# Optimization experiments

Measured on AMD Instinct MI355X. Metric: run time of the kernel, lower is better.

## Reference

```python
import jax, jax.numpy as jnp
import numpy as np

I_DECAY = 0.95
STAG_THRESH = 0.95
MAX_GATE = 0.6
MIN_I_GATE = 0.25
EPS = 1e-12


def setup_inputs() -> dict:
    key = jax.random.key(0)
    ks = jax.random.split(key, 9)
    B, T, D_IN, D_OUT = 4, 2048, 2048, 2048
    x = jax.random.normal(ks[0], (B, T, D_IN), dtype=jnp.float32)
    s = 1.0 / np.sqrt(D_IN)
    Wp = jax.random.uniform(ks[1], (D_IN, D_OUT), jnp.float32, -s, s)
    Wi = jax.random.uniform(ks[2], (D_IN, D_OUT), jnp.float32, -s, s) * 0.3
    Wd = jax.random.uniform(ks[3], (D_IN, D_OUT), jnp.float32, -s, s) * 0.3
    gate_w = jax.random.uniform(ks[4], (D_IN, 3), jnp.float32, -s, s)
    gate_b = jnp.array([0.5, 0.0, 0.0], dtype=jnp.float32)
    kick_vec = jax.random.normal(ks[5], (D_OUT,), dtype=jnp.float32) * 0.01
    kick_w = jax.random.uniform(ks[6], (D_IN, 1), jnp.float32, -s, s)
    kick_b = jnp.full((1,), -2.0, dtype=jnp.float32)
    bias = jnp.zeros((D_OUT,), dtype=jnp.float32)
    return {"x": x, "Wp": Wp, "Wi": Wi, "Wd": Wd, "gate_w": gate_w,
            "gate_b": gate_b, "kick_vec": kick_vec, "kick_w": kick_w,
            "kick_b": kick_b, "bias": bias}


def _ema_integral(x, decay):
    # x: [B,T,D] -> time-major scan; integral[0] = x[0]
    xt = jnp.swapaxes(x, 0, 1)  # [T,B,D]

    def step(carry, xcur):
        new = decay * carry + (1.0 - decay) * xcur
        return new, new

    init = xt[0]
    _, rest = jax.lax.scan(step, init, xt[1:])
    integral = jnp.concatenate([init[None], rest], axis=0)
    return jnp.swapaxes(integral, 0, 1)  # [B,T,D]


def reference(x, Wp, Wi, Wd, gate_w, gate_b, kick_vec, kick_w, kick_b, bias):
    B, T, D = x.shape
    # --- EMA integral (linear recurrence over T) ---
    integral = _ema_integral(x, I_DECAY)

    # --- stagnation-aware derivative ---
    diff = jnp.concatenate(
        [jnp.zeros_like(x[:, :1]), x[:, 1:] - x[:, :-1]], axis=1)
    x_norm = x / jnp.maximum(
        jnp.linalg.norm(x, axis=-1, keepdims=True), EPS)
    cos_sim = jnp.concatenate(
        [jnp.zeros((B, 1), x.dtype),
         jnp.sum(x_norm[:, 1:] * x_norm[:, :-1], axis=-1)], axis=1)  # [B,T]
    stagnation = (cos_sim > STAG_THRESH).astype(x.dtype)
    kick_strength = jax.nn.sigmoid(
        jnp.einsum('btd,do->bto', x, kick_w) + kick_b)[..., 0]  # [B,T]
    derivative = diff + (stagnation * kick_strength)[..., None] * kick_vec

    # --- gates: softmax -> clamp max -> clamp I min -> renormalize ---
    g = jax.nn.softmax(jnp.einsum('btd,dg->btg', x, gate_w) + gate_b, axis=-1)
    g = jnp.minimum(g, MAX_GATE)
    g = g.at[..., 1].set(jnp.maximum(g[..., 1], MIN_I_GATE))
    g = g / jnp.sum(g, axis=-1, keepdims=True)

    out = (g[..., 0:1] * jnp.einsum('btd,do->bto', x, Wp)
           + g[..., 1:2] * jnp.einsum('btd,do->bto', integral, Wi)
           + g[..., 2:3] * jnp.einsum('btd,do->bto', derivative, Wd))
    return out + bias
```

## Files before the change

### kernel.cpp

```cpp
#include <hip/hip_runtime.h>

#define DH 2048
#define TT 2048
#define BB 4
#define MROWS 8192
#define NZ 6144
#define NCH 128
#define LCH 16
#define LAM 0.44012667f
#define LAM2 1.982646e-06f

typedef __attribute__((ext_vector_type(8))) short bf16x8;
typedef __attribute__((ext_vector_type(4))) float f32x4;

__device__ __forceinline__ unsigned short f2bf(float f) {
  union { float f; unsigned int u; } v; v.f = f;
  unsigned int u = v.u;
  return (unsigned short)((u + 0x7FFFu + ((u >> 16) & 1u)) >> 16);
}
__device__ __forceinline__ float bf2f(unsigned short u) {
  union { unsigned int i; float f; } v; v.i = ((unsigned int)u) << 16;
  return v.f;
}
__device__ __forceinline__ void gld16(const unsigned short* g, unsigned short* l) {
  __builtin_amdgcn_global_load_lds((const __attribute__((address_space(1))) void*)g,
                                   (__attribute__((address_space(3))) void*)l, 16, 0, 0);
}

__global__ __launch_bounds__(256) void prep_w(const float* __restrict__ Wp,
                                              const float* __restrict__ Wi,
                                              const float* __restrict__ Wd,
                                              const float* __restrict__ kick_vec,
                                              unsigned short* __restrict__ Wt,
                                              float* __restrict__ kvWd) {
  __shared__ float tile[64][65];
  int bid = blockIdx.x;
  int mat = bid >> 10;
  int t2 = bid & 1023;
  int dt = (t2 >> 5) * 64;
  int ot = (t2 & 31) * 64;
  const float* W = (mat == 0) ? Wp : ((mat == 1) ? Wi : Wd);
  int nbase = mat * DH;
  int tid = threadIdx.x;
  int r = tid >> 4;
  int c4 = (tid & 15) * 4;
#pragma unroll
  for (int i = 0; i < 4; ++i) {
    int rr = r + i * 16;
    float4 v = *(const float4*)&W[(size_t)(dt + rr) * DH + ot + c4];
    tile[rr][c4 + 0] = v.x; tile[rr][c4 + 1] = v.y;
    tile[rr][c4 + 2] = v.z; tile[rr][c4 + 3] = v.w;
  }
  __syncthreads();
  int o = tid >> 3;
  int d8 = (tid & 7) * 8;
#pragma unroll
  for (int pass = 0; pass < 2; ++pass) {
    int oo = o + pass * 32;
    union { unsigned short u[8]; uint4 v; } pk;
#pragma unroll
    for (int i = 0; i < 8; ++i) pk.u[i] = f2bf(tile[d8 + i][oo]);
    *(uint4*)&Wt[(size_t)(nbase + ot + oo) * DH + dt + d8] = pk.v;
  }
  if (mat == 2 && tid < 64) {
    float s = 0.f;
#pragma unroll 8
    for (int dd = 0; dd < 64; ++dd) s += kick_vec[dt + dd] * tile[dd][tid];
    atomicAdd(&kvWd[ot + tid], s);
  }
}

__global__ __launch_bounds__(256) void conv_x(const float* __restrict__ x,
                                              const float* __restrict__ gate_w,
                                              const float* __restrict__ gate_b,
                                              const float* __restrict__ kick_w,
                                              const float* __restrict__ kick_b,
                                              float* __restrict__ rs,
                                              unsigned short* __restrict__ A) {
  int r = blockIdx.x;
  int t = r & (TT - 1);
  const float* xr = x + (size_t)r * DH;
  const float* xq = xr - DH;
  const bool hp = (t != 0);
  int tid = threadIdx.x;
  float a0 = 0, a1 = 0, a2 = 0, ak = 0, axx = 0, apx = 0, app = 0;
#pragma unroll
  for (int it = 0; it < 2; ++it) {
    int d0 = (tid + it * 256) * 4;
    float4 xv = *(const float4*)(xr + d0);
    float4 pv = hp ? *(const float4*)(xq + d0) : make_float4(0.f, 0.f, 0.f, 0.f);
    float4 q0 = *(const float4*)(gate_w + (size_t)d0 * 3);
    float4 q1 = *(const float4*)(gate_w + (size_t)d0 * 3 + 4);
    float4 q2 = *(const float4*)(gate_w + (size_t)d0 * 3 + 8);
    float4 kw = *(const float4*)(kick_w + d0);
    float xa[4] = {xv.x, xv.y, xv.z, xv.w};
    float pa[4] = {pv.x, pv.y, pv.z, pv.w};
    a0 += xa[0] * q0.x + xa[1] * q0.w + xa[2] * q1.z + xa[3] * q2.y;
    a1 += xa[0] * q0.y + xa[1] * q1.x + xa[2] * q1.w + xa[3] * q2.z;
    a2 += xa[0] * q0.z + xa[1] * q1.y + xa[2] * q2.x + xa[3] * q2.w;
    ak += xa[0] * kw.x + xa[1] * kw.y + xa[2] * kw.z + xa[3] * kw.w;
    union { unsigned short u[4]; uint2 v; } pk;
#pragma unroll
    for (int j = 0; j < 4; ++j) {
      axx += xa[j] * xa[j];
      apx += xa[j] * pa[j];
      app += pa[j] * pa[j];
      pk.u[j] = f2bf(xa[j]);
    }
    *(uint2*)&A[(size_t)r * DH + d0] = pk.v;
  }
#pragma unroll
  for (int off = 32; off > 0; off >>= 1) {
    a0 += __shfl_xor(a0, off); a1 += __shfl_xor(a1, off);
    a2 += __shfl_xor(a2, off); ak += __shfl_xor(ak, off);
    axx += __shfl_xor(axx, off); apx += __shfl_xor(apx, off);
    app += __shfl_xor(app, off);
  }
  __shared__ float red[4][7];
  int wv = tid >> 6;
  if ((tid & 63) == 0) {
    red[wv][0] = a0; red[wv][1] = a1; red[wv][2] = a2; red[wv][3] = ak;
    red[wv][4] = axx; red[wv][5] = apx; red[wv][6] = app;
  }
  __syncthreads();
  if (tid == 0) {
    float v[7];
#pragma unroll
    for (int i = 0; i < 7; ++i) v[i] = red[0][i] + red[1][i] + red[2][i] + red[3][i];
    float l0 = v[0] + gate_b[0], l1 = v[1] + gate_b[1], l2 = v[2] + gate_b[2];
    float mx = fmaxf(l0, fmaxf(l1, l2));
    float e0 = expf(l0 - mx), e1 = expf(l1 - mx), e2 = expf(l2 - mx);
    float inv = 1.f / (e0 + e1 + e2);
    float G0 = fminf(e0 * inv, 0.6f);
    float G1 = fminf(e1 * inv, 0.6f);
    float G2 = fminf(e2 * inv, 0.6f);
    G1 = fmaxf(G1, 0.25f);
    float inv2 = 1.f / (G0 + G1 + G2);
    G0 *= inv2; G1 *= inv2; G2 *= inv2;
    float ks = 1.f / (1.f + expf(-(v[3] + kick_b[0])));
    float nn = fmaxf(sqrtf(v[4]), 1e-12f) * fmaxf(sqrtf(v[6]), 1e-12f);
    float cs = hp ? (v[5] / nn) : 0.f;
    float cc = (cs > 0.95f) ? (G2 * ks) : 0.f;
    *(float4*)(rs + (size_t)r * 4) = make_float4(G0, G1, G2, cc);
  }
}

__global__ __launch_bounds__(256) void gemm_kernel(const unsigned short* __restrict__ A,
                                                   const unsigned short* __restrict__ Bt,
                                                   unsigned short* __restrict__ Z) {
  __shared__ __align__(16) unsigned short lA[128 * 64];
  __shared__ __align__(16) unsigned short lB[128 * 64];
  const int tid = threadIdx.x;
  const int wave = tid >> 6, lane = tid & 63;
  const int bid = blockIdx.x;
  const int xcd = bid & 7;
  const int loc = bid >> 3;
  const int mblk = xcd * 8 + (loc & 7);
  const int nblk = loc >> 3;
  const int m0 = mblk * 128, n0 = nblk * 128;

  const int srow = wave * 32 + (lane >> 3);
  const int scol = ((lane & 7) ^ (lane >> 3)) * 8;
  const unsigned short* ga = A + (size_t)(m0 + srow) * DH + scol;
  const unsigned short* gb = Bt + (size_t)(n0 + srow) * DH + scol;
  unsigned short* la = &lA[(wave * 32) * 64];
  unsigned short* lb = &lB[(wave * 32) * 64];

  f32x4 acc[4][4] = {};
  const int arow = ((wave >> 1) * 64 + (lane & 15)) * 64;
  const int brow = ((wave & 1) * 64 + (lane & 15)) * 64;
  const int cbq = lane >> 4;
  const int swz = lane & 7;

  for (int k0 = 0; k0 < DH; k0 += 64) {
#pragma unroll
    for (int j = 0; j < 4; ++j) {
      gld16(ga + k0 + (size_t)j * 8 * DH, la + j * 8 * 64);
      gld16(gb + k0 + (size_t)j * 8 * DH, lb + j * 8 * 64);
    }
    __syncthreads();
#pragma unroll
    for (int kb = 0; kb < 2; ++kb) {
      const int kphys = ((kb * 4 + cbq) ^ swz) * 8;
      bf16x8 av[4], bv[4];
#pragma unroll
      for (int mi = 0; mi < 4; ++mi)
        av[mi] = *(const bf16x8*)&lA[arow + mi * 16 * 64 + kphys];
#pragma unroll
      for (int ni = 0; ni < 4; ++ni)
        bv[ni] = *(const bf16x8*)&lB[brow + ni * 16 * 64 + kphys];
#pragma unroll
      for (int mi = 0; mi < 4; ++mi)
#pragma unroll
        for (int ni = 0; ni < 4; ++ni)
          acc[mi][ni] = __builtin_amdgcn_mfma_f32_16x16x32_bf16(av[mi], bv[ni], acc[mi][ni], 0, 0, 0);
    }
    __syncthreads();
  }

  const int lr = lane >> 4, lc = lane & 15;
  const int mbase = m0 + (wave >> 1) * 64, nbase = n0 + (wave & 1) * 64;
#pragma unroll
  for (int ni = 0; ni < 4; ++ni) {
    const int n = nbase + ni * 16 + lc;
#pragma unroll
    for (int mi = 0; mi < 4; ++mi) {
#pragma unroll
      for (int rg = 0; rg < 4; ++rg) {
        const int m = mbase + mi * 16 + lr * 4 + rg;
        Z[(size_t)m * NZ + n] = f2bf(acc[mi][ni][rg]);
      }
    }
  }
}

__global__ __launch_bounds__(256) void zi_carry(const unsigned short* __restrict__ Z,
                                                unsigned short* __restrict__ cpb) {
  int gid = blockIdx.x * 256 + threadIdx.x;
  int n = (gid & 511) * 4;
  int ch = (gid >> 9) & (NCH - 1);
  int b = gid >> 16;
  const unsigned short* zp = Z + ((size_t)(b * TT + ch * LCH)) * NZ + DH + n;
  float J0, J1, J2, J3;
  int tstart;
  if (ch == 0) {
    union { unsigned short u[4]; uint2 v; } c;
    c.v = *(const uint2*)zp;
    J0 = bf2f(c.u[0]); J1 = bf2f(c.u[1]); J2 = bf2f(c.u[2]); J3 = bf2f(c.u[3]);
    tstart = 1;
  } else {
    J0 = J1 = J2 = J3 = 0.f;
    tstart = 0;
  }
#pragma unroll 4
  for (int t = tstart; t < LCH; ++t) {
    union { unsigned short u[4]; uint2 v; } c;
    c.v = *(const uint2*)(zp + (size_t)t * NZ);
    J0 = 0.95f * J0 + 0.05f * bf2f(c.u[0]);
    J1 = 0.95f * J1 + 0.05f * bf2f(c.u[1]);
    J2 = 0.95f * J2 + 0.05f * bf2f(c.u[2]);
    J3 = 0.95f * J3 + 0.05f * bf2f(c.u[3]);
  }
  union { unsigned short u[4]; uint2 v; } o;
  o.u[0] = f2bf(J0); o.u[1] = f2bf(J1); o.u[2] = f2bf(J2); o.u[3] = f2bf(J3);
  *(uint2*)&cpb[((size_t)b * NCH + ch) * DH + n] = o.v;
}

__global__ __launch_bounds__(256) void zi_p1(unsigned short* __restrict__ cpb,
                                             float* __restrict__ gc) {
  int gid = blockIdx.x * 256 + threadIdx.x;
  int n = (gid & 511) * 4;
  int g = (gid >> 9) & 7;
  int b = gid >> 12;
  float r0 = 0, r1 = 0, r2 = 0, r3 = 0;
#pragma unroll
  for (int j = 0; j < 16; ++j) {
    size_t idx = ((size_t)b * NCH + g * 16 + j) * DH + n;
    union { unsigned short u[4]; uint2 v; } c;
    c.v = *(const uint2*)&cpb[idx];
    float c0 = bf2f(c.u[0]), c1 = bf2f(c.u[1]), c2 = bf2f(c.u[2]), c3 = bf2f(c.u[3]);
    union { unsigned short u[4]; uint2 v; } o;
    o.u[0] = f2bf(r0); o.u[1] = f2bf(r1); o.u[2] = f2bf(r2); o.u[3] = f2bf(r3);
    *(uint2*)&cpb[idx] = o.v;
    r0 = c0 + LAM * r0; r1 = c1 + LAM * r1;
    r2 = c2 + LAM * r2; r3 = c3 + LAM * r3;
  }
  *(float4*)&gc[((size_t)b * 8 + g) * DH + n] = make_float4(r0, r1, r2, r3);
}

__global__ __launch_bounds__(256) void zi_p2(float* __restrict__ gc) {
  int gid = blockIdx.x * 256 + threadIdx.x;
  int n = (gid & 511) * 4;
  int b = gid >> 9;
  float4 run = make_float4(0.f, 0.f, 0.f, 0.f);
#pragma unroll
  for (int g = 0; g < 8; ++g) {
    size_t idx = ((size_t)b * 8 + g) * DH + n;
    float4 old = *(const float4*)&gc[idx];
    *(float4*)&gc[idx] = run;
    run.x = old.x + LAM2 * run.x;
    run.y = old.y + LAM2 * run.y;
    run.z = old.z + LAM2 * run.z;
    run.w = old.w + LAM2 * run.w;
  }
}

__global__ __launch_bounds__(256) void final_combine(const unsigned short* __restrict__ Z,
                                                     const float* __restrict__ rs,
                                                     const unsigned short* __restrict__ cpb,
                                                     const float* __restrict__ gc,
                                                     const float* __restrict__ kvWd,
                                                     const float* __restrict__ bias,
                                                     float* __restrict__ out) {
  int tid = threadIdx.x;
  int n = tid * 8;
  int ch = blockIdx.x & (NCH - 1);
  int b = blockIdx.x >> 7;
  int r0 = b * TT + ch * LCH;
  const unsigned short* zb = Z + (size_t)r0 * NZ + n;
  const bool first_chunk = (ch == 0);

  int g = ch >> 4, j = ch & 15;
  float pw = 1.f;
  for (int i = 0; i < j; ++i) pw *= LAM;
  float Pv[8];
  {
    union { unsigned short u[8]; uint4 v; } c;
    c.v = *(const uint4*)&cpb[((size_t)b * NCH + ch) * DH + n];
    float4 gp0 = *(const float4*)&gc[((size_t)b * 8 + g) * DH + n];
    float4 gp1 = *(const float4*)&gc[((size_t)b * 8 + g) * DH + n + 4];
    float gp[8] = {gp0.x, gp0.y, gp0.z, gp0.w, gp1.x, gp1.y, gp1.z, gp1.w};
#pragma unroll
    for (int i = 0; i < 8; ++i) Pv[i] = bf2f(c.u[i]) + pw * gp[i];
  }
  float kv[8], bz[8];
  {
    float4 k0 = *(const float4*)&kvWd[n], k1 = *(const float4*)&kvWd[n + 4];
    float4 b0 = *(const float4*)&bias[n], b1 = *(const float4*)&bias[n + 4];
    kv[0]=k0.x; kv[1]=k0.y; kv[2]=k0.z; kv[3]=k0.w; kv[4]=k1.x; kv[5]=k1.y; kv[6]=k1.z; kv[7]=k1.w;
    bz[0]=b0.x; bz[1]=b0.y; bz[2]=b0.z; bz[3]=b0.w; bz[4]=b1.x; bz[5]=b1.y; bz[6]=b1.z; bz[7]=b1.w;
  }
  float zdp[8];
  if (!first_chunk) {
    union { unsigned short u[8]; uint4 v; } c;
    c.v = *(const uint4*)(zb - NZ + 2 * DH);
#pragma unroll
    for (int i = 0; i < 8; ++i) zdp[i] = bf2f(c.u[i]);
  } else {
#pragma unroll
    for (int i = 0; i < 8; ++i) zdp[i] = 0.f;
  }
  float J[8];
#pragma unroll
  for (int i = 0; i < 8; ++i) J[i] = 0.f;
  float f = 1.f;
  uint4 cp = *(const uint4*)(zb);
  uint4 ci = *(const uint4*)(zb + DH);
  uint4 cd = *(const uint4*)(zb + 2 * DH);
#pragma unroll
  for (int tau = 0; tau < LCH; ++tau) {
    uint4 np, ni, nd;
    if (tau < LCH - 1) {
      const unsigned short* zn = zb + (size_t)(tau + 1) * NZ;
      np = *(const uint4*)(zn);
      ni = *(const uint4*)(zn + DH);
      nd = *(const uint4*)(zn + 2 * DH);
    }
    float4 gg = *(const float4*)&rs[(size_t)(r0 + tau) * 4];
    union { unsigned short u[8]; uint4 v; } up, ui, ud;
    up.v = cp; ui.v = ci; ud.v = cd;
    const bool vfirst = first_chunk && (tau == 0);
    f *= 0.95f;
    float o[8];
#pragma unroll
    for (int i = 0; i < 8; ++i) {
      float xp = bf2f(up.u[i]), xi = bf2f(ui.u[i]), xd = bf2f(ud.u[i]);
      if (vfirst) J[i] = xi;
      else J[i] = 0.95f * J[i] + 0.05f * xi;
      float I = J[i] + f * Pv[i];
      float diff = vfirst ? 0.f : (xd - zdp[i]);
      o[i] = gg.x * xp + gg.y * I + gg.z * diff + gg.w * kv[i] + bz[i];
      zdp[i] = xd;
    }
    float* orow = out + (size_t)(r0 + tau) * DH + n;
    *(float4*)(orow) = make_float4(o[0], o[1], o[2], o[3]);
    *(float4*)(orow + 4) = make_float4(o[4], o[5], o[6], o[7]);
    cp = np; ci = ni; cd = nd;
  }
}

extern "C" void kernel_launch(void* const* d_in, const int* in_sizes, int n_in,
                              void* d_out, int out_size, void* d_ws, size_t ws_size,
                              hipStream_t stream) {
  const float* x        = (const float*)d_in[0];
  const float* Wp       = (const float*)d_in[1];
  const float* Wi       = (const float*)d_in[2];
  const float* Wd       = (const float*)d_in[3];
  const float* gate_w   = (const float*)d_in[4];
  const float* gate_b   = (const float*)d_in[5];
  const float* kick_vec = (const float*)d_in[6];
  const float* kick_w   = (const float*)d_in[7];
  const float* kick_b   = (const float*)d_in[8];
  const float* bias     = (const float*)d_in[9];
  float* out = (float*)d_out;

  char* ws = (char*)d_ws;
  unsigned short* Wt  = (unsigned short*)(ws + 0);
  unsigned short* Z   = (unsigned short*)(ws + 25165824);
  float* rs   = (float*)(ws + 125829120);
  float* kvWd = (float*)(ws + 125960192);
  unsigned short* cpb = (unsigned short*)(ws + 125968384);
  float* gc   = (float*)(ws + 128065536);
  unsigned short* A = (unsigned short*)d_out;
  (void)ws_size; (void)in_sizes; (void)n_in; (void)out_size;

  hipMemsetAsync(kvWd, 0, DH * sizeof(float), stream);
  prep_w<<<dim3(3072), dim3(256), 0, stream>>>(Wp, Wi, Wd, kick_vec, Wt, kvWd);
  conv_x<<<dim3(8192), dim3(256), 0, stream>>>(x, gate_w, gate_b, kick_w, kick_b, rs, A);
  gemm_kernel<<<dim3(3072), dim3(256), 0, stream>>>(A, Wt, Z);
  zi_carry<<<dim3(1024), dim3(256), 0, stream>>>(Z, cpb);
  zi_p1<<<dim3(64), dim3(256), 0, stream>>>(cpb, gc);
  zi_p2<<<dim3(8), dim3(256), 0, stream>>>(gc);
  final_combine<<<dim3(512), dim3(256), 0, stream>>>(Z, rs, cpb, gc, kvWd, bias, out);
}
```

Baseline: 430.6 us.

## Fuse per-chunk EMA carry into GEMM epilogue and widen scan/combine grids

```diff
diff --git a/kernel.cpp b/kernel.cpp
--- a/kernel.cpp
+++ b/kernel.cpp
@@ -147,7 +147,8 @@
 
 __global__ __launch_bounds__(256) void gemm_kernel(const unsigned short* __restrict__ A,
                                                    const unsigned short* __restrict__ Bt,
-                                                   unsigned short* __restrict__ Z) {
+                                                   unsigned short* __restrict__ Z,
+                                                   unsigned short* __restrict__ cpb) {
   __shared__ __align__(16) unsigned short lA[128 * 64];
   __shared__ __align__(16) unsigned short lB[128 * 64];
   const int tid = threadIdx.x;
@@ -200,6 +201,34 @@
 
   const int lr = lane >> 4, lc = lane & 15;
   const int mbase = m0 + (wave >> 1) * 64, nbase = n0 + (wave & 1) * 64;
+
+  if (nblk >= 16 && nblk < 32) {
+    float w12 = (lr == 3) ? 1.0f : (lr == 2) ? 0.81450625f
+              : (lr == 1) ? 0.66342043f : 0.54036009f;
+    w12 *= 0.05f;
+#pragma unroll
+    for (int mi = 0; mi < 4; ++mi) {
+      const int mrow = mbase + mi * 16;
+      const int bb = mrow >> 11;
+      const int chh = (mrow >> 4) & (NCH - 1);
+      const bool first = (chh == 0);
+#pragma unroll
+      for (int ni = 0; ni < 4; ++ni) {
+        float v0 = acc[mi][ni][0];
+        float s = ((v0 * 0.95f + acc[mi][ni][1]) * 0.95f + acc[mi][ni][2]) * 0.95f
+                  + acc[mi][ni][3];
+        if (first && lr == 0) s += 19.0f * 0.857375f * v0;
+        s *= w12;
+        s += __shfl_xor(s, 16);
+        s += __shfl_xor(s, 32);
+        if (lr == 0) {
+          int nloc = nbase + ni * 16 + lc - 2048;
+          cpb[((size_t)bb * NCH + chh) * DH + nloc] = f2bf(s);
+        }
+      }
+    }
+  }
+
 #pragma unroll
   for (int ni = 0; ni < 4; ++ni) {
     const int n = nbase + ni * 16 + lc;
@@ -214,74 +243,34 @@
   }
 }
 
-__global__ __launch_bounds__(256) void zi_carry(const unsigned short* __restrict__ Z,
-                                                unsigned short* __restrict__ cpb) {
-  int gid = blockIdx.x * 256 + threadIdx.x;
-  int n = (gid & 511) * 4;
-  int ch = (gid >> 9) & (NCH - 1);
-  int b = gid >> 16;
-  const unsigned short* zp = Z + ((size_t)(b * TT + ch * LCH)) * NZ + DH + n;
-  float J0, J1, J2, J3;
-  int tstart;
-  if (ch == 0) {
-    union { unsigned short u[4]; uint2 v; } c;
-    c.v = *(const uint2*)zp;
-    J0 = bf2f(c.u[0]); J1 = bf2f(c.u[1]); J2 = bf2f(c.u[2]); J3 = bf2f(c.u[3]);
-    tstart = 1;
-  } else {
-    J0 = J1 = J2 = J3 = 0.f;
-    tstart = 0;
-  }
-#pragma unroll 4
-  for (int t = tstart; t < LCH; ++t) {
-    union { unsigned short u[4]; uint2 v; } c;
-    c.v = *(const uint2*)(zp + (size_t)t * NZ);
-    J0 = 0.95f * J0 + 0.05f * bf2f(c.u[0]);
-    J1 = 0.95f * J1 + 0.05f * bf2f(c.u[1]);
-    J2 = 0.95f * J2 + 0.05f * bf2f(c.u[2]);
-    J3 = 0.95f * J3 + 0.05f * bf2f(c.u[3]);
-  }
-  union { unsigned short u[4]; uint2 v; } o;
-  o.u[0] = f2bf(J0); o.u[1] = f2bf(J1); o.u[2] = f2bf(J2); o.u[3] = f2bf(J3);
-  *(uint2*)&cpb[((size_t)b * NCH + ch) * DH + n] = o.v;
-}
-
 __global__ __launch_bounds__(256) void zi_p1(unsigned short* __restrict__ cpb,
                                              float* __restrict__ gc) {
   int gid = blockIdx.x * 256 + threadIdx.x;
-  int n = (gid & 511) * 4;
-  int g = (gid >> 9) & 7;
-  int b = gid >> 12;
-  float r0 = 0, r1 = 0, r2 = 0, r3 = 0;
+  int n = gid & (DH - 1);
+  int g = (gid >> 11) & 7;
+  int b = gid >> 14;
+  float run = 0.f;
 #pragma unroll
   for (int j = 0; j < 16; ++j) {
     size_t idx = ((size_t)b * NCH + g * 16 + j) * DH + n;
-    union { unsigned short u[4]; uint2 v; } c;
-    c.v = *(const uint2*)&cpb[idx];
-    float c0 = bf2f(c.u[0]), c1 = bf2f(c.u[1]), c2 = bf2f(c.u[2]), c3 = bf2f(c.u[3]);
-    union { unsigned short u[4]; uint2 v; } o;
-    o.u[0] = f2bf(r0); o.u[1] = f2bf(r1); o.u[2] = f2bf(r2); o.u[3] = f2bf(r3);
-    *(uint2*)&cpb[idx] = o.v;
-    r0 = c0 + LAM * r0; r1 = c1 + LAM * r1;
-    r2 = c2 + LAM * r2; r3 = c3 + LAM * r3;
-  }
-  *(float4*)&gc[((size_t)b * 8 + g) * DH + n] = make_float4(r0, r1, r2, r3);
+    float c = bf2f(cpb[idx]);
+    cpb[idx] = f2bf(run);
+    run = c + LAM * run;
+  }
+  gc[((size_t)b * 8 + g) * DH + n] = run;
 }
 
 __global__ __launch_bounds__(256) void zi_p2(float* __restrict__ gc) {
   int gid = blockIdx.x * 256 + threadIdx.x;
-  int n = (gid & 511) * 4;
-  int b = gid >> 9;
-  float4 run = make_float4(0.f, 0.f, 0.f, 0.f);
+  int n = gid & (DH - 1);
+  int b = gid >> 11;
+  float run = 0.f;
 #pragma unroll
   for (int g = 0; g < 8; ++g) {
     size_t idx = ((size_t)b * 8 + g) * DH + n;
-    float4 old = *(const float4*)&gc[idx];
-    *(float4*)&gc[idx] = run;
-    run.x = old.x + LAM2 * run.x;
-    run.y = old.y + LAM2 * run.y;
-    run.z = old.z + LAM2 * run.z;
-    run.w = old.w + LAM2 * run.w;
+    float old = gc[idx];
+    gc[idx] = run;
+    run = old + LAM2 * run;
   }
 }
 
@@ -293,7 +282,7 @@
                                                      const float* __restrict__ bias,
                                                      float* __restrict__ out) {
   int tid = threadIdx.x;
-  int n = tid * 8;
+  int n = blockIdx.y * 1024 + tid * 4;
   int ch = blockIdx.x & (NCH - 1);
   int b = blockIdx.x >> 7;
   int r0 = b * TT + ch * LCH;
@@ -303,57 +292,56 @@
   int g = ch >> 4, j = ch & 15;
   float pw = 1.f;
   for (int i = 0; i < j; ++i) pw *= LAM;
-  float Pv[8];
+  float Pv[4];
   {
-    union { unsigned short u[8]; uint4 v; } c;
-    c.v = *(const uint4*)&cpb[((size_t)b * NCH + ch) * DH + n];
-    float4 gp0 = *(const float4*)&gc[((size_t)b * 8 + g) * DH + n];
-    float4 gp1 = *(const float4*)&gc[((size_t)b * 8 + g) * DH + n + 4];
-    float gp[8] = {gp0.x, gp0.y, gp0.z, gp0.w, gp1.x, gp1.y, gp1.z, gp1.w};
-#pragma unroll
-    for (int i = 0; i < 8; ++i) Pv[i] = bf2f(c.u[i]) + pw * gp[i];
-  }
-  float kv[8], bz[8];
+    union { unsigned short u[4]; uint2 v; } c;
+    c.v = *(const uint2*)&cpb[((size_t)b * NCH + ch) * DH + n];
+    float4 gp = *(const float4*)&gc[((size_t)b * 8 + g) * DH + n];
+    float gpa[4] = {gp.x, gp.y, gp.z, gp.w};
+#pragma unroll
+    for (int i = 0; i < 4; ++i) Pv[i] = bf2f(c.u[i]) + pw * gpa[i];
+  }
+  float kv[4], bz[4];
   {
-    float4 k0 = *(const float4*)&kvWd[n], k1 = *(const float4*)&kvWd[n + 4];
-    float4 b0 = *(const float4*)&bias[n], b1 = *(const float4*)&bias[n + 4];
-    kv[0]=k0.x; kv[1]=k0.y; kv[2]=k0.z; kv[3]=k0.w; kv[4]=k1.x; kv[5]=k1.y; kv[6]=k1.z; kv[7]=k1.w;
-    bz[0]=b0.x; bz[1]=b0.y; bz[2]=b0.z; bz[3]=b0.w; bz[4]=b1.x; bz[5]=b1.y; bz[6]=b1.z; bz[7]=b1.w;
-  }
-  float zdp[8];
+    float4 k0 = *(const float4*)&kvWd[n];
+    float4 b0 = *(const float4*)&bias[n];
+    kv[0]=k0.x; kv[1]=k0.y; kv[2]=k0.z; kv[3]=k0.w;
+    bz[0]=b0.x; bz[1]=b0.y; bz[2]=b0.z; bz[3]=b0.w;
+  }
+  float zdp[4];
   if (!first_chunk) {
-    union { unsigned short u[8]; uint4 v; } c;
-    c.v = *(const uint4*)(zb - NZ + 2 * DH);
-#pragma unroll
-    for (int i = 0; i < 8; ++i) zdp[i] = bf2f(c.u[i]);
+    union { unsigned short u[4]; uint2 v; } c;
+    c.v = *(const uint2*)(zb - NZ + 2 * DH);
+#pragma unroll
+    for (int i = 0; i < 4; ++i) zdp[i] = bf2f(c.u[i]);
   } else {
 #pragma unroll
-    for (int i = 0; i < 8; ++i) zdp[i] = 0.f;
-  }
-  float J[8];
-#pragma unroll
-  for (int i = 0; i < 8; ++i) J[i] = 0.f;
+    for (int i = 0; i < 4; ++i) zdp[i] = 0.f;
+  }
+  float J[4];
+#pragma unroll
+  for (int i = 0; i < 4; ++i) J[i] = 0.f;
   float f = 1.f;
-  uint4 cp = *(const uint4*)(zb);
-  uint4 ci = *(const uint4*)(zb + DH);
-  uint4 cd = *(const uint4*)(zb + 2 * DH);
+  uint2 cp = *(const uint2*)(zb);
+  uint2 ci = *(const uint2*)(zb + DH);
+  uint2 cd = *(const uint2*)(zb + 2 * DH);
 #pragma unroll
   for (int tau = 0; tau < LCH; ++tau) {
-    uint4 np, ni, nd;
+    uint2 np, ni, nd;
     if (tau < LCH - 1) {
       const unsigned short* zn = zb + (size_t)(tau + 1) * NZ;
-      np = *(const uint4*)(zn);
-      ni = *(const uint4*)(zn + DH);
-      nd = *(const uint4*)(zn + 2 * DH);
+      np = *(const uint2*)(zn);
+      ni = *(const uint2*)(zn + DH);
+      nd = *(const uint2*)(zn + 2 * DH);
     }
     float4 gg = *(const float4*)&rs[(size_t)(r0 + tau) * 4];
-    union { unsigned short u[8]; uint4 v; } up, ui, ud;
+    union { unsigned short u[4]; uint2 v; } up, ui, ud;
     up.v = cp; ui.v = ci; ud.v = cd;
     const bool vfirst = first_chunk && (tau == 0);
     f *= 0.95f;
-    float o[8];
-#pragma unroll
-    for (int i = 0; i < 8; ++i) {
+    float o[4];
+#pragma unroll
+    for (int i = 0; i < 4; ++i) {
       float xp = bf2f(up.u[i]), xi = bf2f(ui.u[i]), xd = bf2f(ud.u[i]);
       if (vfirst) J[i] = xi;
       else J[i] = 0.95f * J[i] + 0.05f * xi;
@@ -362,9 +350,7 @@
       o[i] = gg.x * xp + gg.y * I + gg.z * diff + gg.w * kv[i] + bz[i];
       zdp[i] = xd;
     }
-    float* orow = out + (size_t)(r0 + tau) * DH + n;
-    *(float4*)(orow) = make_float4(o[0], o[1], o[2], o[3]);
-    *(float4*)(orow + 4) = make_float4(o[4], o[5], o[6], o[7]);
+    *(float4*)(out + (size_t)(r0 + tau) * DH + n) = make_float4(o[0], o[1], o[2], o[3]);
     cp = np; ci = ni; cd = nd;
   }
 }
@@ -397,9 +383,8 @@
   hipMemsetAsync(kvWd, 0, DH * sizeof(float), stream);
   prep_w<<<dim3(3072), dim3(256), 0, stream>>>(Wp, Wi, Wd, kick_vec, Wt, kvWd);
   conv_x<<<dim3(8192), dim3(256), 0, stream>>>(x, gate_w, gate_b, kick_w, kick_b, rs, A);
-  gemm_kernel<<<dim3(3072), dim3(256), 0, stream>>>(A, Wt, Z);
-  zi_carry<<<dim3(1024), dim3(256), 0, stream>>>(Z, cpb);
-  zi_p1<<<dim3(64), dim3(256), 0, stream>>>(cpb, gc);
-  zi_p2<<<dim3(8), dim3(256), 0, stream>>>(gc);
-  final_combine<<<dim3(512), dim3(256), 0, stream>>>(Z, rs, cpb, gc, kvWd, bias, out);
-}
+  gemm_kernel<<<dim3(3072), dim3(256), 0, stream>>>(A, Wt, Z, cpb);
+  zi_p1<<<dim3(256), dim3(256), 0, stream>>>(cpb, gc);
+  zi_p2<<<dim3(32), dim3(256), 0, stream>>>(gc);
+  final_combine<<<dim3(512, 2), dim3(256), 0, stream>>>(Z, rs, cpb, gc, kvWd, bias, out);
+}
```

Measured after the change: 419.8 us. 1.03x faster.
